# Optimization experiments

Measured on AMD Instinct MI355X. Metric: run time of the kernel, lower is better.

Reference implementation:

```python
import jax, jax.numpy as jnp
import numpy as np

D = 1024
H = 4
HD = D // H
B = 256
L = 64
DILATIONS = (1, 4, 8, 16)


def setup_inputs() -> dict:
    key = jax.random.key(0)
    ks = jax.random.split(key, 12)
    s = 1.0 / np.sqrt(D)
    return {
        "x": jax.random.normal(ks[0], (B, D), jnp.float32),
        "hist": jax.random.normal(ks[1], (L, B, D), jnp.float32),
        "Wq": jax.random.normal(ks[2], (D, D), jnp.float32) * s,
        "bq": jnp.zeros((D,), jnp.float32),
        "Wk": jax.random.normal(ks[3], (D, D), jnp.float32) * s,
        "bk": jnp.zeros((D,), jnp.float32),
        "Wv": jax.random.normal(ks[4], (D, D), jnp.float32) * s,
        "bv": jnp.zeros((D,), jnp.float32),
        "Wo": jax.random.normal(ks[5], (D, D), jnp.float32) * s,
        "bo": jnp.zeros((D,), jnp.float32),
        "dil_w": jnp.full((len(DILATIONS),), 1.0 / len(DILATIONS), jnp.float32),
        "gamma": jnp.ones((D,), jnp.float32),
        "beta": jnp.zeros((D,), jnp.float32),
    }


def reference(x, hist, Wq, bq, Wk, bk, Wv, bv, Wo, bo, dil_w, gamma, beta):
    scale = 1.0 / np.sqrt(HD)
    q = (x @ Wq + bq).reshape(B, H, HD)  # (B, H, HD)
    attended = []
    for d in DILATIONS:
        # history frames at stride d, concatenated along dim 0 (faithful to torch.cat)
        frames = hist[::d].reshape(-1, D)              # (T', D), T' = ceil(L/d)*B
        k = (frames @ Wk + bk).reshape(-1, H, HD)      # (T', H, HD)
        v = (frames @ Wv + bv).reshape(-1, H, HD)
        s = jnp.einsum('bhd,thd->bht', q, k) * scale   # (B, H, T')
        a = jax.nn.softmax(s, axis=-1)
        attended.append(jnp.einsum('bht,thd->bhd', a, v).reshape(B, D))
    w = jax.nn.softmax(dil_w, axis=0)
    combined = sum(w[i] * attended[i] for i in range(len(DILATIONS)))
    y = x + combined @ Wo + bo
    mu = jnp.mean(y, axis=-1, keepdims=True)
    var = jnp.var(y, axis=-1, keepdims=True)
    return (y - mu) / jnp.sqrt(var + 1e-5) * gamma + beta
```

## Files before the change

kernel.cpp:

```cpp
#include <hip/hip_runtime.h>


#define DD    1024
#define TALL  16384

typedef _Float16 half8  __attribute__((ext_vector_type(8)));
typedef _Float16 half4v __attribute__((ext_vector_type(4)));
typedef float    floatx4 __attribute__((ext_vector_type(4)));
typedef unsigned int u32;

static const size_t OFF_WOT  = 0;
static const size_t OFF_WV16 = 2097152;
static const size_t OFF_WK16 = 4194304;
static const size_t OFF_WQ16 = 6291456;
static const size_t OFF_XB   = 8388608;
static const size_t OFF_G    = 8912896;
static const size_t OFF_WVOT = 11010048;
static const size_t OFF_WQKT = 19398656;
static const size_t OFF_BVWO = 27787264;
static const size_t OFF_BQK  = 27791360;
static const size_t OFF_PHR  = 27807744;
static const size_t OFF_OPP  = 29904896;
static const size_t OFF_HB   = 38293504;
static const size_t OFF_PHP  = OFF_HB;
static const size_t OFF_HT   = 71848960;
static const size_t OFF_S    = 105403392;

__device__ __forceinline__ void gl_lds16(const void* g, void* l) {
  __builtin_amdgcn_global_load_lds((const __attribute__((address_space(1))) u32*)g,
                                   (__attribute__((address_space(3))) u32*)l, 16, 0, 0);
}

__global__ void prep_kernel(const float* __restrict__ Wo, const float* __restrict__ Wv,
                            const float* __restrict__ Wk, const float* __restrict__ Wq,
                            const float* __restrict__ x, const float* __restrict__ hist,
                            _Float16* __restrict__ WoT, _Float16* __restrict__ Wv16,
                            _Float16* __restrict__ Wk16, _Float16* __restrict__ Wq16,
                            _Float16* __restrict__ xb, _Float16* __restrict__ histb,
                            _Float16* __restrict__ histT) {
  int bid = blockIdx.x, tid = threadIdx.x;
  if (bid < 1024) {
    int k0 = (bid & 31) * 32, n0 = (bid >> 5) * 32;
    __shared__ float t32[32][33];
    int tx = tid & 31, ty = tid >> 5;
#pragma unroll
    for (int i = 0; i < 4; i++) {
      int r = ty + i * 8;
      t32[r][tx] = Wo[(size_t)(k0 + r) * DD + n0 + tx];
    }
    __syncthreads();
#pragma unroll
    for (int i = 0; i < 4; i++) {
      int r = ty + i * 8;
      WoT[(size_t)(n0 + r) * DD + k0 + tx] = (_Float16)t32[tx][r];
    }
  } else if (bid < 4352) {
    const float* src; _Float16* dst; size_t i;
    if (bid < 2048)      { src = Wv; dst = Wv16; i = (size_t)(bid - 1024) * 256 + tid; }
    else if (bid < 3072) { src = Wk; dst = Wk16; i = (size_t)(bid - 2048) * 256 + tid; }
    else if (bid < 4096) { src = Wq; dst = Wq16; i = (size_t)(bid - 3072) * 256 + tid; }
    else                 { src = x;  dst = xb;   i = (size_t)(bid - 4096) * 256 + tid; }
    float4 v = ((const float4*)src)[i];
    half4v h = {(_Float16)v.x, (_Float16)v.y, (_Float16)v.z, (_Float16)v.w};
    *(half4v*)(dst + 4 * i) = h;
  } else {
    int tb = bid - 4352;
    int t0 = (tb & 255) * 64, f0 = (tb >> 8) * 64;
    __shared__ _Float16 lt[64][72];
    int r = tid >> 2, c0 = (tid & 3) * 16;
    half8 s0, s1;
#pragma unroll
    for (int i = 0; i < 4; i++) {
      float4 v = *(const float4*)&hist[(size_t)(t0 + r) * 1024 + f0 + c0 + i * 4];
      half4v h = {(_Float16)v.x, (_Float16)v.y, (_Float16)v.z, (_Float16)v.w};
      *(half4v*)&lt[r][c0 + i * 4] = h;
      if (i < 2) { s0[i*4]=h[0]; s0[i*4+1]=h[1]; s0[i*4+2]=h[2]; s0[i*4+3]=h[3]; }
      else { s1[(i-2)*4]=h[0]; s1[(i-2)*4+1]=h[1]; s1[(i-2)*4+2]=h[2]; s1[(i-2)*4+3]=h[3]; }
    }
    *(half8*)&histb[(size_t)(t0 + r) * 1024 + f0 + c0] = s0;
    *(half8*)&histb[(size_t)(t0 + r) * 1024 + f0 + c0 + 8] = s1;
    __syncthreads();
    int fr = tid >> 2, tc0 = (tid & 3) * 16;
    half8 o0, o1;
#pragma unroll
    for (int j = 0; j < 8; j++) { o0[j] = lt[tc0 + j][fr]; o1[j] = lt[tc0 + 8 + j][fr]; }
    *(half8*)&histT[(size_t)(f0 + fr) * TALL + t0 + tc0] = o0;
    *(half8*)&histT[(size_t)(f0 + fr) * TALL + t0 + tc0 + 8] = o1;
  }
}

__device__ __forceinline__ void gemm_core(const _Float16* __restrict__ A, size_t lda,
                                          const _Float16* __restrict__ B, size_t ldb,
                                          int kIters, _Float16* As, _Float16* Bs,
                                          int tid, floatx4 acc[4][4]) {
  int lane = tid & 63, w = tid >> 6;
  int l15 = lane & 15, quad = lane >> 4;
  int wm = (w >> 1) * 64, wn = (w & 1) * 64;
  int swz = ((tid & 3) ^ ((tid >> 3) & 3)) * 8;
  int pch = (quad ^ ((l15 >> 1) & 3)) * 8;
  const char* gA0 = (const char*)(A + (size_t)(tid >> 2) * lda + swz);
  const char* gA1 = (const char*)(A + ((size_t)(tid >> 2) + 64) * lda + swz);
  const char* gB0 = (const char*)(B + (size_t)(tid >> 2) * ldb + swz);
  const char* gB1 = (const char*)(B + ((size_t)(tid >> 2) + 64) * ldb + swz);
  _Float16* lA = As + w * 512;
  _Float16* lB = Bs + w * 512;
#define GC_STAGE(buf, k)                                    \
  do {                                                      \
    size_t off_ = (size_t)(k) * 64;                         \
    gl_lds16(gA0 + off_, lA + (buf) * 4096);                \
    gl_lds16(gA1 + off_, lA + (buf) * 4096 + 2048);         \
    gl_lds16(gB0 + off_, lB + (buf) * 4096);                \
    gl_lds16(gB1 + off_, lB + (buf) * 4096 + 2048);         \
  } while (0)
#define GC_STEP(buf, k)                                                       \
  do {                                                                        \
    if ((k) + 1 < kIters) asm volatile("s_waitcnt vmcnt(4)" ::: "memory");    \
    else                  asm volatile("s_waitcnt vmcnt(0)" ::: "memory");    \
    asm volatile("s_barrier" ::: "memory");                                   \
    const _Float16* Ac_ = As + (buf) * 4096;                                  \
    const _Float16* Bc_ = Bs + (buf) * 4096;                                  \
    half8 a_[4];                                                              \
    _Pragma("unroll")                                                         \
    for (int mi = 0; mi < 4; mi++)                                            \
      a_[mi] = *(const half8*)&Ac_[(wm + mi * 16 + l15) * 32 + pch];          \
    _Pragma("unroll")                                                         \
    for (int ni = 0; ni < 4; ni++) {                                          \
      half8 b8_ = *(const half8*)&Bc_[(wn + ni * 16 + l15) * 32 + pch];       \
      _Pragma("unroll")                                                       \
      for (int mi = 0; mi < 4; mi++)                                          \
        acc[mi][ni] = __builtin_amdgcn_mfma_f32_16x16x32_f16(a_[mi], b8_,     \
                                                             acc[mi][ni], 0, 0, 0); \
    }                                                                         \
    asm volatile("s_waitcnt lgkmcnt(0)" ::: "memory");                        \
    asm volatile("s_barrier" ::: "memory");                                   \
    if ((k) + 2 < kIters) GC_STAGE(buf, (k) + 2);                             \
  } while (0)
  GC_STAGE(0, 0);
  GC_STAGE(1, 1);
  for (int kk = 0; kk < kIters; kk += 2) {
    GC_STEP(0, kk);
    GC_STEP(1, kk + 1);
  }
#undef GC_STEP
#undef GC_STAGE
}

template <bool OUTF32>
__launch_bounds__(256, 3)
__global__ void gemm_f16_kernel(const _Float16* __restrict__ A, size_t lda, size_t aoffz,
                                const _Float16* __restrict__ B, size_t ldb, size_t boffz,
                                int kIters, const float* __restrict__ bias, size_t biasoffz,
                                float scale, void* __restrict__ C, size_t ldc, size_t coffz) {
  __shared__ __align__(16) _Float16 As[8192];
  __shared__ __align__(16) _Float16 Bs[8192];
  int tid = threadIdx.x;
  const _Float16* Ab = A + aoffz * blockIdx.z + (size_t)(blockIdx.y * 128) * lda;
  const _Float16* Bb = B + boffz * blockIdx.z + (size_t)(blockIdx.x * 128) * ldb;
  floatx4 acc[4][4];
  floatx4 zero = {0.f, 0.f, 0.f, 0.f};
#pragma unroll
  for (int a = 0; a < 4; a++)
#pragma unroll
    for (int b = 0; b < 4; b++) acc[a][b] = zero;
  gemm_core(Ab, lda, Bb, ldb, kIters, As, Bs, tid, acc);
  int lane = tid & 63, w = tid >> 6;
  int l15 = lane & 15, quad = lane >> 4;
  int wm = (w >> 1) * 64, wn = (w & 1) * 64;
#pragma unroll
  for (int mi = 0; mi < 4; mi++)
#pragma unroll
    for (int ni = 0; ni < 4; ni++) {
      int colg = blockIdx.x * 128 + wn + ni * 16 + l15;
      float bv = bias ? bias[biasoffz * blockIdx.z + colg] : 0.f;
#pragma unroll
      for (int r = 0; r < 4; r++) {
        int rowg = blockIdx.y * 128 + wm + mi * 16 + quad * 4 + r;
        float v = (acc[mi][ni][r] + bv) * scale;
        size_t idx = coffz * blockIdx.z + (size_t)rowg * ldc + colg;
        if (OUTF32) ((float*)C)[idx] = v;
        else ((_Float16*)C)[idx] = (_Float16)v;
      }
    }
}

__launch_bounds__(256, 3)
__global__ void wpack_kernel(const _Float16* __restrict__ WoT, const _Float16* __restrict__ Wv16,
                             const _Float16* __restrict__ Wk16, const _Float16* __restrict__ Wq16,
                             const float* __restrict__ bv, const float* __restrict__ bq,
                             _Float16* __restrict__ WVOT, _Float16* __restrict__ WQKT,
                             float* __restrict__ bvwo, float* __restrict__ bqk) {
  __shared__ __align__(16) _Float16 As[8192];
  __shared__ __align__(16) _Float16 Bs[8192];
  int bid = blockIdx.x, tid = threadIdx.x;
  if (bid < 512) {
    bool isQK = bid >= 256;
    int g = bid & 255;
    int x = g & 7, y = (g >> 3) & 7, z = g >> 6;
    const _Float16* A = isQK ? Wk16 : WoT;
    const _Float16* B = isQK ? Wq16 : Wv16;
    const _Float16* Ab = A + 256 * z + (size_t)(y * 128) * 1024;
    const _Float16* Bb = B + 256 * z + (size_t)(x * 128) * 1024;
    floatx4 acc[4][4];
    floatx4 zero = {0.f, 0.f, 0.f, 0.f};
#pragma unroll
    for (int a = 0; a < 4; a++)
#pragma unroll
      for (int b = 0; b < 4; b++) acc[a][b] = zero;
    gemm_core(Ab, 1024, Bb, 1024, 8, As, Bs, tid, acc);
    float scale = isQK ? 0.0625f : 1.0f;
    _Float16* C = isQK ? WQKT : WVOT;
    size_t ldc = isQK ? 1024 : 4096;
    size_t zoff = isQK ? (size_t)1048576 * z : (size_t)1024 * z;
    int lane = tid & 63, w = tid >> 6;
    int l15 = lane & 15, quad = lane >> 4;
    int wm = (w >> 1) * 64, wn = (w & 1) * 64;
#pragma unroll
    for (int mi = 0; mi < 4; mi++)
#pragma unroll
      for (int ni = 0; ni < 4; ni++) {
        int col = x * 128 + wn + ni * 16 + l15;
#pragma unroll
        for (int r = 0; r < 4; r++) {
          int row = y * 128 + wm + mi * 16 + quad * 4 + r;
          C[zoff + (size_t)row * ldc + col] = (_Float16)(acc[mi][ni][r] * scale);
        }
      }
  } else if (bid < 516) {
    int j = (bid - 512) * 256 + tid;
    const half8* row = (const half8*)(WoT + (size_t)j * 1024);
    float a = 0.f;
    for (int c = 0; c < 128; c++) {
      half8 w8 = row[c];
#pragma unroll
      for (int e = 0; e < 8; e++) a += bv[c * 8 + e] * (float)w8[e];
    }
    bvwo[j] = a;
  } else {
    int idx = (bid - 516) * 256 + tid;
    int h = idx >> 10, f = idx & 1023;
    const _Float16* row = Wk16 + (size_t)f * 1024 + h * 256;
    float a = 0.f;
    for (int n = 0; n < 256; n++) a += bq[h * 256 + n] * (float)row[n];
    bqk[idx] = a * 0.0625f;
  }
}

__launch_bounds__(256, 4)
__global__ void gemm_s_kernel(const _Float16* __restrict__ G, const _Float16* __restrict__ histb,
                              _Float16* __restrict__ S) {
  __shared__ __align__(16) _Float16 As[8192];
  __shared__ __align__(16) _Float16 Bs[8192];
  int bid = blockIdx.x, tid = threadIdx.x;
  int b7 = bid & 7, rr = bid >> 3;
  int x = ((rr & 15) << 3) | b7;
  int yh = rr >> 4;
  int y = yh & 1, h = yh >> 1;
  const _Float16* Ab = G + (size_t)h * 262144 + (size_t)(y * 128) * 1024;
  const _Float16* Bb = histb + (size_t)(x * 128) * 1024;
  floatx4 acc[4][4];
  floatx4 zero = {0.f, 0.f, 0.f, 0.f};
#pragma unroll
  for (int a = 0; a < 4; a++)
#pragma unroll
    for (int b = 0; b < 4; b++) acc[a][b] = zero;
  gemm_core(Ab, 1024, Bb, 1024, 32, As, Bs, tid, acc);
  int lane = tid & 63, w = tid >> 6;
  int l15 = lane & 15, quad = lane >> 4;
  int wm = (w >> 1) * 64, wn = (w & 1) * 64;
#pragma unroll
  for (int mi = 0; mi < 4; mi++)
#pragma unroll
    for (int ni = 0; ni < 4; ni++) {
      int col = x * 128 + wn + ni * 16 + l15;
#pragma unroll
      for (int r = 0; r < 4; r++) {
        int row = y * 128 + wm + mi * 16 + quad * 4 + r;
        S[(size_t)h * 4194304 + (size_t)row * TALL + col] = (_Float16)acc[mi][ni][r];
      }
    }
}

__global__ void softmax_kernel(_Float16* __restrict__ S, const float* __restrict__ dil_w) {
  int r = blockIdx.x, tid = threadIdx.x;
  _Float16* row = S + (size_t)r * TALL;
  int lane = tid & 63;
  float ef[8][8];
  float es[8];
  __shared__ float Zf[64];
  __shared__ float Zd[4];
  __shared__ float cf[64];
#pragma unroll
  for (int i = 0; i < 8; i++) {
    half8 v = *(const half8*)&row[((size_t)i * 256 + tid) * 8];
    float s = 0.f;
#pragma unroll
    for (int j = 0; j < 8; j++) { float e = __expf((float)v[j]); ef[i][j] = e; s += e; }
#pragma unroll
    for (int off = 1; off <= 16; off <<= 1) s += __shfl_xor(s, off, 64);
    es[i] = s;
  }
  if ((lane & 31) == 0) {
    int half = tid >> 5;
#pragma unroll
    for (int i = 0; i < 8; i++) Zf[i * 8 + half] = es[i];
  }
  __syncthreads();
  if (tid < 4) {
    int step = 1 << (tid + (tid ? 1 : 0));
    float z = 0.f;
    for (int f = 0; f < 64; f += step) z += Zf[f];
    Zd[tid] = z;
  }
  __syncthreads();
  if (tid < 64) {
    float w0 = dil_w[0], w1 = dil_w[1], w2 = dil_w[2], w3 = dil_w[3];
    float wmx = fmaxf(fmaxf(w0, w1), fmaxf(w2, w3));
    float e0 = __expf(w0 - wmx), e1 = __expf(w1 - wmx), e2 = __expf(w2 - wmx), e3 = __expf(w3 - wmx);
    float wsum = e0 + e1 + e2 + e3;
    float c = (e0 / wsum) / Zd[0];
    if ((tid & 3) == 0) c += (e1 / wsum) / Zd[1];
    if ((tid & 7) == 0) c += (e2 / wsum) / Zd[2];
    if ((tid & 15) == 0) c += (e3 / wsum) / Zd[3];
    cf[tid] = c * 256.0f;
  }
  __syncthreads();
#pragma unroll
  for (int i = 0; i < 8; i++) {
    float c = cf[i * 8 + (tid >> 5)];
    half8 o;
#pragma unroll
    for (int j = 0; j < 8; j++) o[j] = (_Float16)(ef[i][j] * c);
    *(half8*)&row[((size_t)i * 256 + tid) * 8] = o;
  }
}

__launch_bounds__(256, 3)
__global__ void gemm_ph_kernel(const _Float16* __restrict__ P, const _Float16* __restrict__ histT,
                               float* __restrict__ part) {
  __shared__ __align__(16) _Float16 As[8192];
  __shared__ __align__(16) _Float16 Bs[8192];
  int bid = blockIdx.x, tid = threadIdx.x;
  int sp = bid & 7, rr = bid >> 3;
  int x = rr & 7, yh = rr >> 3;
  int y = yh & 1, h = yh >> 1;
  const _Float16* Ab = P + (size_t)h * 4194304 + (size_t)(y * 128) * TALL + sp * 2048;
  const _Float16* Bb = histT + (size_t)(x * 128) * TALL + sp * 2048;
  floatx4 acc[4][4];
  floatx4 zero = {0.f, 0.f, 0.f, 0.f};
#pragma unroll
  for (int a = 0; a < 4; a++)
#pragma unroll
    for (int b = 0; b < 4; b++) acc[a][b] = zero;
  gemm_core(Ab, TALL, Bb, TALL, 64, As, Bs, tid, acc);
  int lane = tid & 63, w = tid >> 6;
  int l15 = lane & 15, quad = lane >> 4;
  int wm = (w >> 1) * 64, wn = (w & 1) * 64;
#pragma unroll
  for (int mi = 0; mi < 4; mi++)
#pragma unroll
    for (int ni = 0; ni < 4; ni++) {
      int k = x * 128 + wn + ni * 16 + l15;
#pragma unroll
      for (int r = 0; r < 4; r++) {
        int q = y * 128 + wm + mi * 16 + quad * 4 + r;
        part[(size_t)(h * 8 + sp) * 262144 + (size_t)q * 1024 + k] = acc[mi][ni][r];
      }
    }
}

__global__ void reduce_ph_kernel(const float* __restrict__ part, _Float16* __restrict__ PHred) {
  size_t e4 = ((size_t)blockIdx.x * 256 + threadIdx.x) * 4;
  int q = (int)(e4 >> 12);
  int hk = (int)(e4 & 4095);
  int h = hk >> 10, k = hk & 1023;
  float4 s = {0.f, 0.f, 0.f, 0.f};
#pragma unroll
  for (int sp = 0; sp < 8; sp++) {
    float4 p = *(const float4*)&part[(size_t)(h * 8 + sp) * 262144 + (size_t)q * 1024 + k];
    s.x += p.x; s.y += p.y; s.z += p.z; s.w += p.w;
  }
  half4v o = {(_Float16)s.x, (_Float16)s.y, (_Float16)s.z, (_Float16)s.w};
  *(half4v*)&PHred[e4] = o;
}

__global__ void ln_kernel(const float* __restrict__ x, const float* __restrict__ part2,
                          const float* __restrict__ bo, const float* __restrict__ bvwo,
                          const float* __restrict__ gamma, const float* __restrict__ beta,
                          float* __restrict__ out) {
  int b = blockIdx.x, t = threadIdx.x;
  __shared__ float red[8];
  float y[4];
  float sum = 0.f, sq = 0.f;
#pragma unroll
  for (int i = 0; i < 4; i++) {
    int j = t + i * 256;
    float v = x[(size_t)b * 1024 + j] + bo[j] + bvwo[j];
#pragma unroll
    for (int z = 0; z < 8; z++) v += part2[(size_t)z * 262144 + (size_t)b * 1024 + j];
    y[i] = v;
    sum += v;
    sq += v * v;
  }
#pragma unroll
  for (int off = 1; off < 64; off <<= 1) {
    sum += __shfl_xor(sum, off, 64);
    sq += __shfl_xor(sq, off, 64);
  }
  int w = t >> 6, lane = t & 63;
  if (lane == 0) { red[w] = sum; red[4 + w] = sq; }
  __syncthreads();
  sum = red[0] + red[1] + red[2] + red[3];
  sq = red[4] + red[5] + red[6] + red[7];
  float mu = sum * (1.f / 1024.f);
  float var = sq * (1.f / 1024.f) - mu * mu;
  float inv = rsqrtf(var + 1e-5f);
#pragma unroll
  for (int i = 0; i < 4; i++) {
    int j = t + i * 256;
    out[(size_t)b * 1024 + j] = (y[i] - mu) * inv * gamma[j] + beta[j];
  }
}

extern "C" void kernel_launch(void* const* d_in, const int* in_sizes, int n_in,
                              void* d_out, int out_size, void* d_ws, size_t ws_size,
                              hipStream_t stream) {
  const float* x     = (const float*)d_in[0];
  const float* hist  = (const float*)d_in[1];
  const float* Wq    = (const float*)d_in[2];
  const float* bq    = (const float*)d_in[3];
  const float* Wk    = (const float*)d_in[4];
  const float* Wv    = (const float*)d_in[6];
  const float* bv    = (const float*)d_in[7];
  const float* Wo    = (const float*)d_in[8];
  const float* bo    = (const float*)d_in[9];
  const float* dil_w = (const float*)d_in[10];
  const float* gamma = (const float*)d_in[11];
  const float* beta  = (const float*)d_in[12];
  char* ws = (char*)d_ws;

  _Float16* WoT   = (_Float16*)(ws + OFF_WOT);
  _Float16* Wv16  = (_Float16*)(ws + OFF_WV16);
  _Float16* Wk16  = (_Float16*)(ws + OFF_WK16);
  _Float16* Wq16  = (_Float16*)(ws + OFF_WQ16);
  _Float16* xb    = (_Float16*)(ws + OFF_XB);
  _Float16* G     = (_Float16*)(ws + OFF_G);
  _Float16* WVOT  = (_Float16*)(ws + OFF_WVOT);
  _Float16* WQKT  = (_Float16*)(ws + OFF_WQKT);
  float* bvwo     = (float*)(ws + OFF_BVWO);
  float* bqk      = (float*)(ws + OFF_BQK);
  _Float16* PHred = (_Float16*)(ws + OFF_PHR);
  float* oppart   = (float*)(ws + OFF_OPP);
  _Float16* histb = (_Float16*)(ws + OFF_HB);
  float* phpart   = (float*)(ws + OFF_PHP);
  _Float16* histT = (_Float16*)(ws + OFF_HT);
  _Float16* Sb    = (_Float16*)(ws + OFF_S);

  prep_kernel<<<dim3(8448), 256, 0, stream>>>(Wo, Wv, Wk, Wq, x, hist,
                                              WoT, Wv16, Wk16, Wq16, xb, histb, histT);
  wpack_kernel<<<dim3(532), 256, 0, stream>>>(WoT, Wv16, Wk16, Wq16, bv, bq,
                                              WVOT, WQKT, bvwo, bqk);
  gemm_f16_kernel<false><<<dim3(8, 2, 4), 256, 0, stream>>>(
      xb, 1024, 0, WQKT, 1024, 1048576, 32, bqk, 1024, 1.0f, (void*)G, 1024, 262144);
  gemm_s_kernel<<<dim3(1024), 256, 0, stream>>>(G, histb, Sb);
  softmax_kernel<<<dim3(1024), 256, 0, stream>>>(Sb, dil_w);
  gemm_ph_kernel<<<dim3(512), 256, 0, stream>>>(Sb, histT, phpart);
  reduce_ph_kernel<<<dim3(1024), 256, 0, stream>>>(phpart, PHred);
  gemm_f16_kernel<true><<<dim3(8, 2, 8), 256, 0, stream>>>(
      PHred, 4096, 512, WVOT, 4096, 512, 16, nullptr, 0, 1.0f / 256.0f,
      (void*)oppart, 1024, 262144);
  ln_kernel<<<dim3(256), 256, 0, stream>>>(x, oppart, bo, bvwo, gamma, beta, (float*)d_out);
}
```

Baseline: 323.2 us.

## Use 256x256 tiles with 4-stage pipeline for S and PH GEMMs, 14-way split-K

New measurement: 342.3 us. +5.9%, slower.

```diff
diff --git a/kernel.cpp b/kernel.cpp
--- a/kernel.cpp
+++ b/kernel.cpp
@@ -22,9 +22,15 @@
 static const size_t OFF_PHR  = 27807744;
 static const size_t OFF_OPP  = 29904896;
 static const size_t OFF_HB   = 38293504;
-static const size_t OFF_PHP  = OFF_HB;
 static const size_t OFF_HT   = 71848960;
 static const size_t OFF_S    = 105403392;
+
+__device__ __forceinline__ size_t chunk_off(int g) {
+  if (g < 2) return (size_t)g * 4194304;
+  if (g < 4) return 19398656 + (size_t)(g - 2) * 4194304;
+  if (g < 6) return 29904896 + (size_t)(g - 4) * 4194304;
+  return 38293504 + (size_t)(g - 6) * 4194304;
+}
 
 __device__ __forceinline__ void gl_lds16(const void* g, void* l) {
   __builtin_amdgcn_global_load_lds((const __attribute__((address_space(1))) u32*)g,
@@ -145,6 +151,69 @@
 #undef GC_STAGE
 }
 
+__device__ __forceinline__ void gemm256_core(const _Float16* __restrict__ A, size_t lda,
+                                             const _Float16* __restrict__ B, size_t ldb,
+                                             int nT, _Float16* As, _Float16* Bs,
+                                             int tid, floatx4 acc[8][4]) {
+  int lane = tid & 63, w = tid >> 6;
+  int l15 = lane & 15, quad = lane >> 4;
+  int wr = w >> 2, wc = w & 3;
+  int pch = (quad ^ ((l15 >> 1) & 3)) * 8;
+  int srow = tid >> 2;
+  int schunk = (tid & 3) ^ ((tid >> 3) & 3);
+  const char* gA0 = (const char*)(A + (size_t)srow * lda + schunk * 8);
+  const char* gA1 = (const char*)(A + (size_t)(srow + 128) * lda + schunk * 8);
+  const char* gB0 = (const char*)(B + (size_t)srow * ldb + schunk * 8);
+  const char* gB1 = (const char*)(B + (size_t)(srow + 128) * ldb + schunk * 8);
+  _Float16* lA = As + w * 512;
+  _Float16* lB = Bs + w * 512;
+#define ST256(buf, t)                                         \
+  do { size_t o_ = (size_t)(t) * 64;                          \
+    gl_lds16(gA0 + o_, lA + (buf) * 8192);                    \
+    gl_lds16(gA1 + o_, lA + (buf) * 8192 + 4096);             \
+    gl_lds16(gB0 + o_, lB + (buf) * 8192);                    \
+    gl_lds16(gB1 + o_, lB + (buf) * 8192 + 4096);             \
+  } while (0)
+  ST256(0, 0);
+  ST256(1, 1);
+  for (int t = 0; t < nT; ++t) {
+    int buf = t & 3;
+    if (t + 1 < nT) asm volatile("s_waitcnt vmcnt(4)" ::: "memory");
+    else            asm volatile("s_waitcnt vmcnt(0)" ::: "memory");
+    asm volatile("s_barrier" ::: "memory");
+    if (t + 2 < nT) ST256((t + 2) & 3, t + 2);
+    const _Float16* Ac = As + buf * 8192;
+    const _Float16* Bc = Bs + buf * 8192;
+    half8 b8[4];
+#pragma unroll
+    for (int ni = 0; ni < 4; ni++)
+      b8[ni] = *(const half8*)&Bc[(wc * 64 + ni * 16 + l15) * 32 + pch];
+    half8 a8[4];
+#pragma unroll
+    for (int mi = 0; mi < 4; mi++)
+      a8[mi] = *(const half8*)&Ac[(wr * 128 + mi * 16 + l15) * 32 + pch];
+    __builtin_amdgcn_s_setprio(1);
+#pragma unroll
+    for (int mi = 0; mi < 4; mi++)
+#pragma unroll
+      for (int ni = 0; ni < 4; ni++)
+        acc[mi][ni] = __builtin_amdgcn_mfma_f32_16x16x32_f16(a8[mi], b8[ni], acc[mi][ni], 0, 0, 0);
+    __builtin_amdgcn_s_setprio(0);
+#pragma unroll
+    for (int mi = 0; mi < 4; mi++)
+      a8[mi] = *(const half8*)&Ac[(wr * 128 + 64 + mi * 16 + l15) * 32 + pch];
+    __builtin_amdgcn_s_setprio(1);
+#pragma unroll
+    for (int mi = 0; mi < 4; mi++)
+#pragma unroll
+      for (int ni = 0; ni < 4; ni++)
+        acc[4 + mi][ni] = __builtin_amdgcn_mfma_f32_16x16x32_f16(a8[mi], b8[ni], acc[4 + mi][ni], 0, 0, 0);
+    __builtin_amdgcn_s_setprio(0);
+    asm volatile("s_waitcnt lgkmcnt(0)" ::: "memory");
+  }
+#undef ST256
+}
+
 template <bool OUTF32>
 __launch_bounds__(256, 3)
 __global__ void gemm_f16_kernel(const _Float16* __restrict__ A, size_t lda, size_t aoffz,
@@ -245,39 +314,38 @@
   }
 }
 
-__launch_bounds__(256, 4)
-__global__ void gemm_s_kernel(const _Float16* __restrict__ G, const _Float16* __restrict__ histb,
-                              _Float16* __restrict__ S) {
-  __shared__ __align__(16) _Float16 As[8192];
-  __shared__ __align__(16) _Float16 Bs[8192];
+__launch_bounds__(512, 2)
+__global__ void gemm256_s_kernel(const _Float16* __restrict__ G, const _Float16* __restrict__ histb,
+                                 _Float16* __restrict__ S) {
+  __shared__ __align__(16) _Float16 As[32768];
+  __shared__ __align__(16) _Float16 Bs[32768];
   int bid = blockIdx.x, tid = threadIdx.x;
-  int b7 = bid & 7, rr = bid >> 3;
-  int x = ((rr & 15) << 3) | b7;
-  int yh = rr >> 4;
-  int y = yh & 1, h = yh >> 1;
-  const _Float16* Ab = G + (size_t)h * 262144 + (size_t)(y * 128) * 1024;
-  const _Float16* Bb = histb + (size_t)(x * 128) * 1024;
-  floatx4 acc[4][4];
+  int h = bid >> 6, nt = bid & 63;
+  const _Float16* Ab = G + (size_t)h * 262144;
+  const _Float16* Bb = histb + (size_t)(nt * 256) * 1024;
+  floatx4 acc[8][4];
   floatx4 zero = {0.f, 0.f, 0.f, 0.f};
 #pragma unroll
-  for (int a = 0; a < 4; a++)
+  for (int a = 0; a < 8; a++)
 #pragma unroll
     for (int b = 0; b < 4; b++) acc[a][b] = zero;
-  gemm_core(Ab, 1024, Bb, 1024, 32, As, Bs, tid, acc);
+  gemm256_core(Ab, 1024, Bb, 1024, 32, As, Bs, tid, acc);
   int lane = tid & 63, w = tid >> 6;
   int l15 = lane & 15, quad = lane >> 4;
-  int wm = (w >> 1) * 64, wn = (w & 1) * 64;
-#pragma unroll
-  for (int mi = 0; mi < 4; mi++)
-#pragma unroll
-    for (int ni = 0; ni < 4; ni++) {
-      int col = x * 128 + wn + ni * 16 + l15;
-#pragma unroll
-      for (int r = 0; r < 4; r++) {
-        int row = y * 128 + wm + mi * 16 + quad * 4 + r;
-        S[(size_t)h * 4194304 + (size_t)row * TALL + col] = (_Float16)acc[mi][ni][r];
+  int wr = w >> 2, wc = w & 3;
+#pragma unroll
+  for (int mh = 0; mh < 2; mh++)
+#pragma unroll
+    for (int mi = 0; mi < 4; mi++)
+#pragma unroll
+      for (int ni = 0; ni < 4; ni++) {
+        int col = nt * 256 + wc * 64 + ni * 16 + l15;
+#pragma unroll
+        for (int r = 0; r < 4; r++) {
+          int row = wr * 128 + mh * 64 + mi * 16 + quad * 4 + r;
+          S[(size_t)h * 4194304 + (size_t)row * TALL + col] = (_Float16)acc[mh * 4 + mi][ni][r];
+        }
       }
-    }
 }
 
 __global__ void softmax_kernel(_Float16* __restrict__ S, const float* __restrict__ dil_w) {
@@ -334,50 +402,53 @@
   }
 }
 
-__launch_bounds__(256, 3)
-__global__ void gemm_ph_kernel(const _Float16* __restrict__ P, const _Float16* __restrict__ histT,
-                               float* __restrict__ part) {
-  __shared__ __align__(16) _Float16 As[8192];
-  __shared__ __align__(16) _Float16 Bs[8192];
+__launch_bounds__(512, 2)
+__global__ void gemm256_ph_kernel(const _Float16* __restrict__ P, const _Float16* __restrict__ histT,
+                                  char* __restrict__ ws) {
+  __shared__ __align__(16) _Float16 As[32768];
+  __shared__ __align__(16) _Float16 Bs[32768];
   int bid = blockIdx.x, tid = threadIdx.x;
-  int sp = bid & 7, rr = bid >> 3;
-  int x = rr & 7, yh = rr >> 3;
-  int y = yh & 1, h = yh >> 1;
-  const _Float16* Ab = P + (size_t)h * 4194304 + (size_t)(y * 128) * TALL + sp * 2048;
-  const _Float16* Bb = histT + (size_t)(x * 128) * TALL + sp * 2048;
-  floatx4 acc[4][4];
+  int g = bid >> 4, hn = bid & 15;
+  int h = hn >> 2, nt = hn & 3;
+  int start, nT;
+  if (g < 8) { start = g * 37; nT = 37; }
+  else       { start = 296 + (g - 8) * 36; nT = 36; }
+  const _Float16* Ab = P + (size_t)h * 4194304 + (size_t)start * 32;
+  const _Float16* Bb = histT + (size_t)(nt * 256) * TALL + (size_t)start * 32;
+  floatx4 acc[8][4];
   floatx4 zero = {0.f, 0.f, 0.f, 0.f};
 #pragma unroll
-  for (int a = 0; a < 4; a++)
+  for (int a = 0; a < 8; a++)
 #pragma unroll
     for (int b = 0; b < 4; b++) acc[a][b] = zero;
-  gemm_core(Ab, TALL, Bb, TALL, 64, As, Bs, tid, acc);
+  gemm256_core(Ab, TALL, Bb, TALL, nT, As, Bs, tid, acc);
+  float* chunk = (float*)(ws + chunk_off(g));
   int lane = tid & 63, w = tid >> 6;
   int l15 = lane & 15, quad = lane >> 4;
-  int wm = (w >> 1) * 64, wn = (w & 1) * 64;
-#pragma unroll
-  for (int mi = 0; mi < 4; mi++)
-#pragma unroll
-    for (int ni = 0; ni < 4; ni++) {
-      int k = x * 128 + wn + ni * 16 + l15;
-#pragma unroll
-      for (int r = 0; r < 4; r++) {
-        int q = y * 128 + wm + mi * 16 + quad * 4 + r;
-        part[(size_t)(h * 8 + sp) * 262144 + (size_t)q * 1024 + k] = acc[mi][ni][r];
+  int wr = w >> 2, wc = w & 3;
+#pragma unroll
+  for (int mh = 0; mh < 2; mh++)
+#pragma unroll
+    for (int mi = 0; mi < 4; mi++)
+#pragma unroll
+      for (int ni = 0; ni < 4; ni++) {
+        int col = h * 1024 + nt * 256 + wc * 64 + ni * 16 + l15;
+#pragma unroll
+        for (int r = 0; r < 4; r++) {
+          int row = wr * 128 + mh * 64 + mi * 16 + quad * 4 + r;
+          chunk[(size_t)row * 4096 + col] = acc[mh * 4 + mi][ni][r];
+        }
       }
-    }
-}
-
-__global__ void reduce_ph_kernel(const float* __restrict__ part, _Float16* __restrict__ PHred) {
+}
+
+__global__ void reduce_ph_kernel(const char* __restrict__ ws, _Float16* __restrict__ PHred) {
   size_t e4 = ((size_t)blockIdx.x * 256 + threadIdx.x) * 4;
-  int q = (int)(e4 >> 12);
-  int hk = (int)(e4 & 4095);
-  int h = hk >> 10, k = hk & 1023;
   float4 s = {0.f, 0.f, 0.f, 0.f};
 #pragma unroll
-  for (int sp = 0; sp < 8; sp++) {
-    float4 p = *(const float4*)&part[(size_t)(h * 8 + sp) * 262144 + (size_t)q * 1024 + k];
-    s.x += p.x; s.y += p.y; s.z += p.z; s.w += p.w;
+  for (int g = 0; g < 14; g++) {
+    const float* p = (const float*)(ws + chunk_off(g));
+    float4 v = *(const float4*)&p[e4];
+    s.x += v.x; s.y += v.y; s.z += v.z; s.w += v.w;
   }
   half4v o = {(_Float16)s.x, (_Float16)s.y, (_Float16)s.z, (_Float16)s.w};
   *(half4v*)&PHred[e4] = o;
@@ -451,7 +522,6 @@
   _Float16* PHred = (_Float16*)(ws + OFF_PHR);
   float* oppart   = (float*)(ws + OFF_OPP);
   _Float16* histb = (_Float16*)(ws + OFF_HB);
-  float* phpart   = (float*)(ws + OFF_PHP);
   _Float16* histT = (_Float16*)(ws + OFF_HT);
   _Float16* Sb    = (_Float16*)(ws + OFF_S);
 
@@ -461,10 +531,10 @@
                                               WVOT, WQKT, bvwo, bqk);
   gemm_f16_kernel<false><<<dim3(8, 2, 4), 256, 0, stream>>>(
       xb, 1024, 0, WQKT, 1024, 1048576, 32, bqk, 1024, 1.0f, (void*)G, 1024, 262144);
-  gemm_s_kernel<<<dim3(1024), 256, 0, stream>>>(G, histb, Sb);
+  gemm256_s_kernel<<<dim3(256), 512, 0, stream>>>(G, histb, Sb);
   softmax_kernel<<<dim3(1024), 256, 0, stream>>>(Sb, dil_w);
-  gemm_ph_kernel<<<dim3(512), 256, 0, stream>>>(Sb, histT, phpart);
-  reduce_ph_kernel<<<dim3(1024), 256, 0, stream>>>(phpart, PHred);
+  gemm256_ph_kernel<<<dim3(224), 512, 0, stream>>>(Sb, histT, ws);
+  reduce_ph_kernel<<<dim3(1024), 256, 0, stream>>>(ws, PHred);
   gemm_f16_kernel<true><<<dim3(8, 2, 8), 256, 0, stream>>>(
       PHred, 4096, 512, WVOT, 4096, 512, 16, nullptr, 0, 1.0f / 256.0f,
       (void*)oppart, 1024, 262144);
```
